# Kernel optimization log

Hardware: AMD Instinct MI355X
Metric: run time of the kernel (lower is better)

## Reference

```python
import jax, jax.numpy as jnp
import numpy as np

B, C, H, W = 4, 32, 128, 256
EPS = 1e-5  # BatchNorm eps


def _conv1x1_bn(x, w, b, gamma, beta, mean, var):
    # x: [B,C,H,W]; 1x1 conv == channel matmul, fused with eval-mode BatchNorm
    y = jnp.einsum('bchw,oc->bohw', x, w) + b[None, :, None, None]
    scale = gamma / jnp.sqrt(var + EPS)
    shift = beta - mean * scale
    return y * scale[None, :, None, None] + shift[None, :, None, None]


def setup_inputs() -> dict:
    key = jax.random.key(0)
    ks = jax.random.split(key, 15)
    d = {
        'x_left': jax.random.normal(ks[0], (B, C, H, W), jnp.float32),
        'x_right': jax.random.normal(ks[1], (B, C, H, W), jnp.float32),
        'cost': jax.random.normal(ks[2], (2, B, H, W, W), jnp.float32),
        'q_w': jax.random.normal(ks[3], (C, C), jnp.float32),
        'q_b': jax.random.normal(ks[4], (C,), jnp.float32),
        'q_gamma': jax.random.uniform(ks[5], (C,), jnp.float32),
        'q_beta': jax.random.normal(ks[6], (C,), jnp.float32),
        'q_mean': jax.random.normal(ks[7], (C,), jnp.float32),
        'q_var': jax.random.uniform(ks[8], (C,), jnp.float32),
        'k_w': jax.random.normal(ks[9], (C, C), jnp.float32),
        'k_b': jax.random.normal(ks[10], (C,), jnp.float32),
        'k_gamma': jax.random.uniform(ks[11], (C,), jnp.float32),
        'k_beta': jax.random.normal(ks[12], (C,), jnp.float32),
        'k_mean': jax.random.normal(ks[13], (C,), jnp.float32),
        'k_var': jax.random.uniform(ks[14], (C,), jnp.float32),
    }
    return d


def reference(x_left, x_right, cost, q_w, q_b, q_gamma, q_beta, q_mean, q_var,
              k_w, k_b, k_gamma, k_beta, k_mean, k_var):
    b, c, h, w = x_left.shape
    cr = w // 3  # clamped_range

    # band masks: right2left keeps 0 <= i-j < cr (lower band); left2right keeps 0 <= j-i < cr
    idx = jnp.arange(w)
    diff = idx[:, None] - idx[None, :]  # [W,W] = i - j
    low_band = ((diff >= 0) & (diff < cr)).astype(x_left.dtype)
    up_band = low_band.T

    # right-to-left: Q from left, K from right
    q_l = jnp.transpose(_conv1x1_bn(x_left, q_w, q_b, q_gamma, q_beta, q_mean, q_var), (0, 2, 3, 1))   # [B,H,W,C]
    k_r = jnp.transpose(_conv1x1_bn(x_right, k_w, k_b, k_gamma, k_beta, k_mean, k_var), (0, 2, 3, 1))  # [B,H,W,C]
    s_r2l = jnp.einsum('bhic,bhjc->bhij', q_l, k_r) / c  # [B,H,W,W]
    cost_r2l = s_r2l * low_band + cost[0]

    # left-to-right: Q from right, K from left
    q_r = jnp.transpose(_conv1x1_bn(x_right, q_w, q_b, q_gamma, q_beta, q_mean, q_var), (0, 2, 3, 1))
    k_l = jnp.transpose(_conv1x1_bn(x_left, k_w, k_b, k_gamma, k_beta, k_mean, k_var), (0, 2, 3, 1))
    s_l2r = jnp.einsum('bhic,bhjc->bhij', q_r, k_l) / c
    cost_l2r = s_l2r * up_band + cost[1]

    # original returns (x_left + fea_left, x_right + fea_right, (r2l, l2r)) with fea == x
    return (x_left * 2.0, x_right * 2.0, cost_r2l, cost_l2r)
```

## Files before the change

### kernel.cpp

```cpp
#include <hip/hip_runtime.h>

#define BB 4
#define CC 32
#define HH 128
#define WW 256
#define CR 85
#define EPSF 1e-5f

#define O1_OFF 4194304
#define O2_OFF 8388608
#define COST1 33554432

typedef __attribute__((ext_vector_type(8))) short bf16x8;
typedef __attribute__((ext_vector_type(4))) float f32x4;
typedef __attribute__((ext_vector_type(4))) float f4v;

static __device__ __forceinline__ unsigned short f2bf(float f) {
    unsigned u = __float_as_uint(f);
    unsigned r = (u + 0x7FFFu + ((u >> 16) & 1u)) >> 16;
    return (unsigned short)r;
}

__global__ __launch_bounds__(256, 3)
void pab_fused_one(const float* __restrict__ x_left, const float* __restrict__ x_right,
                   const float* __restrict__ cost,
                   const float* __restrict__ q_w, const float* __restrict__ q_b,
                   const float* __restrict__ q_gamma, const float* __restrict__ q_beta,
                   const float* __restrict__ q_mean, const float* __restrict__ q_var,
                   const float* __restrict__ k_w, const float* __restrict__ k_b,
                   const float* __restrict__ k_gamma, const float* __restrict__ k_beta,
                   const float* __restrict__ k_mean, const float* __restrict__ k_var,
                   float* __restrict__ out)
{
    __shared__ unsigned short Qs[WW * CC];
    __shared__ unsigned short Ks[WW * CC];
    __shared__ char smem[32 * 132 * 4];
    float* Sb = (float*)smem;
    float (*wqs)[CC] = (float(*)[CC])smem;
    float (*wks)[CC] = (float(*)[CC])(smem + 4096);
    float* bqs = (float*)(smem + 8192);
    float* bks = (float*)(smem + 8320);
    float* sqs = (float*)(smem + 8448);
    float* sks = (float*)(smem + 8576);

    const int t   = threadIdx.x;
    const int dir = blockIdx.x >> 9;
    const int bh  = blockIdx.x & 511;
    const int b = bh >> 7, h = bh & 127;

    if (t < CC) {
        float qs_ = q_gamma[t] * rsqrtf(q_var[t] + EPSF);
        float ks_ = k_gamma[t] * rsqrtf(k_var[t] + EPSF);
        sqs[t] = qs_; sks[t] = ks_;
        bqs[t] = q_b[t] * qs_ + q_beta[t] - q_mean[t] * qs_;
        bks[t] = k_b[t] * ks_ + k_beta[t] - k_mean[t] * ks_;
    }
    __syncthreads();
    for (int r = t; r < CC * CC; r += 256) {
        int o = r >> 5, c = r & 31;
        wqs[c][o] = q_w[r] * sqs[o];
        wks[c][o] = k_w[r] * sks[o];
    }
    __syncthreads();

    const float* xq = dir ? x_right : x_left;
    const float* xk = dir ? x_left  : x_right;
    float* outq = out + (dir ? O1_OFF : 0);
    const int xbase = (b * CC * HH + h) * WW + t;

    {
        float q[CC];
        #pragma unroll
        for (int o = 0; o < CC; ++o) q[o] = bqs[o];
        #pragma unroll 4
        for (int c = 0; c < CC; ++c) {
            int idx = xbase + c * (HH * WW);
            float xv = xq[idx];
            __builtin_nontemporal_store(2.0f * xv, outq + idx);
            #pragma unroll
            for (int o = 0; o < CC; ++o) q[o] += xv * wqs[c][o];
        }
        unsigned short* qdst = Qs + t * CC;
        #pragma unroll
        for (int g = 0; g < 4; ++g) {
            uint4 v;
            v.x = f2bf(q[8*g+0]) | ((unsigned)f2bf(q[8*g+1]) << 16);
            v.y = f2bf(q[8*g+2]) | ((unsigned)f2bf(q[8*g+3]) << 16);
            v.z = f2bf(q[8*g+4]) | ((unsigned)f2bf(q[8*g+5]) << 16);
            v.w = f2bf(q[8*g+6]) | ((unsigned)f2bf(q[8*g+7]) << 16);
            ((uint4*)qdst)[g] = v;
        }
    }
    {
        float k[CC];
        #pragma unroll
        for (int o = 0; o < CC; ++o) k[o] = bks[o];
        #pragma unroll 4
        for (int c = 0; c < CC; ++c) {
            float xv = xk[xbase + c * (HH * WW)];
            #pragma unroll
            for (int o = 0; o < CC; ++o) k[o] += xv * wks[c][o];
        }
        unsigned short* kdst = Ks + t * CC;
        #pragma unroll
        for (int g = 0; g < 4; ++g) {
            uint4 v;
            v.x = f2bf(k[8*g+0]) | ((unsigned)f2bf(k[8*g+1]) << 16);
            v.y = f2bf(k[8*g+2]) | ((unsigned)f2bf(k[8*g+3]) << 16);
            v.z = f2bf(k[8*g+4]) | ((unsigned)f2bf(k[8*g+5]) << 16);
            v.w = f2bf(k[8*g+6]) | ((unsigned)f2bf(k[8*g+7]) << 16);
            ((uint4*)kdst)[g] = v;
        }
    }
    __syncthreads();

    const float* csrc = cost + (size_t)dir * COST1 + (size_t)bh * (WW * WW);
    float* odst = out + O2_OFF + (size_t)dir * COST1 + (size_t)bh * (WW * WW);
    const int rowlane = t >> 6;
    const int c4 = 4 * (t & 63);
    const int w = t >> 6, lane = t & 63;
    const int quad = lane >> 4, l16 = lane & 15;
    const float inv32 = 1.0f / 32.0f;

    for (int tile = 0; tile < 8; ++tile) {
        const int i0 = tile * 32;
        const int wbase = dir ? i0 : (i0 - 96);

        f4v vbuf[8];
        #pragma unroll
        for (int p = 0; p < 8; ++p) {
            int rl = 4 * p + rowlane;
            vbuf[p] = __builtin_nontemporal_load((const f4v*)(csrc + (i0 + rl) * WW + c4));
        }

        bf16x8 qf[2], kf[2];
        #pragma unroll
        for (int mt = 0; mt < 2; ++mt)
            qf[mt] = *(const bf16x8*)(Qs + (i0 + 16 * mt + l16) * CC + quad * 8);
        #pragma unroll
        for (int nt = 0; nt < 2; ++nt) {
            int col = wbase + 32 * w + 16 * nt + l16;
            bf16x8 kv = {};
            if (col >= 0 && col < WW)
                kv = *(const bf16x8*)(Ks + col * CC + quad * 8);
            kf[nt] = kv;
        }

        f32x4 acc[2][2] = {};
        #pragma unroll
        for (int mt = 0; mt < 2; ++mt)
            #pragma unroll
            for (int nt = 0; nt < 2; ++nt)
                acc[mt][nt] = __builtin_amdgcn_mfma_f32_16x16x32_bf16(
                    qf[mt], kf[nt], acc[mt][nt], 0, 0, 0);

        __syncthreads();

        #pragma unroll
        for (int mt = 0; mt < 2; ++mt)
            #pragma unroll
            for (int nt = 0; nt < 2; ++nt) {
                int cl = 32 * w + 16 * nt + l16;
                #pragma unroll
                for (int r = 0; r < 4; ++r) {
                    int row = 16 * mt + quad * 4 + r;
                    Sb[row * 132 + cl] = acc[mt][nt][r];
                }
            }
        __syncthreads();

        const int lc = c4 - wbase;
        const bool inwin = (lc >= 0 && lc < 128);
        #pragma unroll
        for (int p = 0; p < 8; ++p) {
            int rl = 4 * p + rowlane;
            int i = i0 + rl;
            f4v v = vbuf[p];
            if (inwin) {
                const f4v s = *(const f4v*)(Sb + rl * 132 + lc);
                int d0 = dir ? (c4 + 0 - i) : (i - c4 - 0);
                int d1 = dir ? (c4 + 1 - i) : (i - c4 - 1);
                int d2 = dir ? (c4 + 2 - i) : (i - c4 - 2);
                int d3 = dir ? (c4 + 3 - i) : (i - c4 - 3);
                if (d0 >= 0 && d0 < CR) v[0] += s[0] * inv32;
                if (d1 >= 0 && d1 < CR) v[1] += s[1] * inv32;
                if (d2 >= 0 && d2 < CR) v[2] += s[2] * inv32;
                if (d3 >= 0 && d3 < CR) v[3] += s[3] * inv32;
            }
            __builtin_nontemporal_store(v, (f4v*)(odst + (size_t)i * WW + c4));
        }
    }
}

extern "C" void kernel_launch(void* const* d_in, const int* in_sizes, int n_in,
                              void* d_out, int out_size, void* d_ws, size_t ws_size,
                              hipStream_t stream) {
    const float* x_left  = (const float*)d_in[0];
    const float* x_right = (const float*)d_in[1];
    const float* cost    = (const float*)d_in[2];
    const float* q_w     = (const float*)d_in[3];
    const float* q_b     = (const float*)d_in[4];
    const float* q_gamma = (const float*)d_in[5];
    const float* q_beta  = (const float*)d_in[6];
    const float* q_mean  = (const float*)d_in[7];
    const float* q_var   = (const float*)d_in[8];
    const float* k_w     = (const float*)d_in[9];
    const float* k_b     = (const float*)d_in[10];
    const float* k_gamma = (const float*)d_in[11];
    const float* k_beta  = (const float*)d_in[12];
    const float* k_mean  = (const float*)d_in[13];
    const float* k_var   = (const float*)d_in[14];
    float* out = (float*)d_out;

    pab_fused_one<<<dim3(1024), dim3(256), 0, stream>>>(
        x_left, x_right, cost,
        q_w, q_b, q_gamma, q_beta, q_mean, q_var,
        k_w, k_b, k_gamma, k_beta, k_mean, k_var,
        out);
}
```

Before: 531.4 us.

## Split each row across two blocks, prefetch cost tiles, swizzle score buffer

Each (dir,b,h) row is split into two blocks, each covering 128 query rows, which doubles the grid to 2048 blocks and raises the occupancy hint to 4. The first cost tile is loaded before the Q/K projections and the next tile is prefetched inside the store loop, so global loads overlap with compute. Q projection work is split across thread halves with 16 outputs each. The score buffer uses an XOR swizzle instead of padding to avoid LDS bank conflicts. The cost is that the K projection for the full row is now recomputed by both halves.

```diff
diff --git a/kernel.cpp b/kernel.cpp
--- a/kernel.cpp
+++ b/kernel.cpp
@@ -21,20 +21,22 @@
     return (unsigned short)r;
 }
 
-__global__ __launch_bounds__(256, 3)
-void pab_fused_one(const float* __restrict__ x_left, const float* __restrict__ x_right,
-                   const float* __restrict__ cost,
-                   const float* __restrict__ q_w, const float* __restrict__ q_b,
-                   const float* __restrict__ q_gamma, const float* __restrict__ q_beta,
-                   const float* __restrict__ q_mean, const float* __restrict__ q_var,
-                   const float* __restrict__ k_w, const float* __restrict__ k_b,
-                   const float* __restrict__ k_gamma, const float* __restrict__ k_beta,
-                   const float* __restrict__ k_mean, const float* __restrict__ k_var,
-                   float* __restrict__ out)
+#define SBS(r, c) ((r) * 128 + (((((c) >> 2) ^ ((r) & 7)) << 2) | ((c) & 3)))
+
+__global__ __launch_bounds__(256, 4)
+void pab_fused_half(const float* __restrict__ x_left, const float* __restrict__ x_right,
+                    const float* __restrict__ cost,
+                    const float* __restrict__ q_w, const float* __restrict__ q_b,
+                    const float* __restrict__ q_gamma, const float* __restrict__ q_beta,
+                    const float* __restrict__ q_mean, const float* __restrict__ q_var,
+                    const float* __restrict__ k_w, const float* __restrict__ k_b,
+                    const float* __restrict__ k_gamma, const float* __restrict__ k_beta,
+                    const float* __restrict__ k_mean, const float* __restrict__ k_var,
+                    float* __restrict__ out)
 {
-    __shared__ unsigned short Qs[WW * CC];
+    __shared__ unsigned short Qs[128 * CC];
     __shared__ unsigned short Ks[WW * CC];
-    __shared__ char smem[32 * 132 * 4];
+    __shared__ char smem[32 * 128 * 4];
     float* Sb = (float*)smem;
     float (*wqs)[CC] = (float(*)[CC])smem;
     float (*wks)[CC] = (float(*)[CC])(smem + 4096);
@@ -43,10 +45,25 @@
     float* sqs = (float*)(smem + 8448);
     float* sks = (float*)(smem + 8576);
 
-    const int t   = threadIdx.x;
-    const int dir = blockIdx.x >> 9;
-    const int bh  = blockIdx.x & 511;
+    const int t    = threadIdx.x;
+    const int bx   = blockIdx.x;
+    const int dir  = bx >> 10;
+    const int bh   = (bx >> 1) & 511;
+    const int half = bx & 1;
     const int b = bh >> 7, h = bh & 127;
+    const int ibase = half * 128;
+
+    const float* csrc = cost + (size_t)dir * COST1 + (size_t)bh * (WW * WW);
+    float* odst = out + O2_OFF + (size_t)dir * COST1 + (size_t)bh * (WW * WW);
+    const int rowlane = t >> 6;
+    const int c4 = 4 * (t & 63);
+
+    f4v vbuf[8];
+    #pragma unroll
+    for (int p = 0; p < 8; ++p) {
+        int rl = 4 * p + rowlane;
+        vbuf[p] = __builtin_nontemporal_load((const f4v*)(csrc + (ibase + rl) * WW + c4));
+    }
 
     if (t < CC) {
         float qs_ = q_gamma[t] * rsqrtf(q_var[t] + EPSF);
@@ -66,38 +83,15 @@
     const float* xq = dir ? x_right : x_left;
     const float* xk = dir ? x_left  : x_right;
     float* outq = out + (dir ? O1_OFF : 0);
-    const int xbase = (b * CC * HH + h) * WW + t;
 
     {
-        float q[CC];
-        #pragma unroll
-        for (int o = 0; o < CC; ++o) q[o] = bqs[o];
+        float k[CC];
+        #pragma unroll
+        for (int o = 0; o < CC; ++o) k[o] = bks[o];
+        const int xkbase = (b * CC * HH + h) * WW + t;
         #pragma unroll 4
         for (int c = 0; c < CC; ++c) {
-            int idx = xbase + c * (HH * WW);
-            float xv = xq[idx];
-            __builtin_nontemporal_store(2.0f * xv, outq + idx);
-            #pragma unroll
-            for (int o = 0; o < CC; ++o) q[o] += xv * wqs[c][o];
-        }
-        unsigned short* qdst = Qs + t * CC;
-        #pragma unroll
-        for (int g = 0; g < 4; ++g) {
-            uint4 v;
-            v.x = f2bf(q[8*g+0]) | ((unsigned)f2bf(q[8*g+1]) << 16);
-            v.y = f2bf(q[8*g+2]) | ((unsigned)f2bf(q[8*g+3]) << 16);
-            v.z = f2bf(q[8*g+4]) | ((unsigned)f2bf(q[8*g+5]) << 16);
-            v.w = f2bf(q[8*g+6]) | ((unsigned)f2bf(q[8*g+7]) << 16);
-            ((uint4*)qdst)[g] = v;
-        }
-    }
-    {
-        float k[CC];
-        #pragma unroll
-        for (int o = 0; o < CC; ++o) k[o] = bks[o];
-        #pragma unroll 4
-        for (int c = 0; c < CC; ++c) {
-            float xv = xk[xbase + c * (HH * WW)];
+            float xv = xk[xkbase + c * (HH * WW)];
             #pragma unroll
             for (int o = 0; o < CC; ++o) k[o] += xv * wks[c][o];
         }
@@ -112,31 +106,48 @@
             ((uint4*)kdst)[g] = v;
         }
     }
+
+    {
+        const int lpx = t & 127;
+        const int oh  = t >> 7;
+        const int ob  = oh * 16;
+        float q[16];
+        #pragma unroll
+        for (int o = 0; o < 16; ++o) q[o] = bqs[ob + o];
+        const int xqbase = (b * CC * HH + h) * WW + ibase + lpx;
+        #pragma unroll 4
+        for (int c = 0; c < CC; ++c) {
+            float xv = xq[xqbase + c * (HH * WW)];
+            if (t < 128)
+                __builtin_nontemporal_store(2.0f * xv, outq + xqbase + c * (HH * WW));
+            #pragma unroll
+            for (int o = 0; o < 16; ++o) q[o] += xv * wqs[c][ob + o];
+        }
+        unsigned short* qdst = Qs + lpx * CC + ob;
+        #pragma unroll
+        for (int g = 0; g < 2; ++g) {
+            uint4 v;
+            v.x = f2bf(q[8*g+0]) | ((unsigned)f2bf(q[8*g+1]) << 16);
+            v.y = f2bf(q[8*g+2]) | ((unsigned)f2bf(q[8*g+3]) << 16);
+            v.z = f2bf(q[8*g+4]) | ((unsigned)f2bf(q[8*g+5]) << 16);
+            v.w = f2bf(q[8*g+6]) | ((unsigned)f2bf(q[8*g+7]) << 16);
+            ((uint4*)qdst)[g] = v;
+        }
+    }
     __syncthreads();
 
-    const float* csrc = cost + (size_t)dir * COST1 + (size_t)bh * (WW * WW);
-    float* odst = out + O2_OFF + (size_t)dir * COST1 + (size_t)bh * (WW * WW);
-    const int rowlane = t >> 6;
-    const int c4 = 4 * (t & 63);
     const int w = t >> 6, lane = t & 63;
     const int quad = lane >> 4, l16 = lane & 15;
     const float inv32 = 1.0f / 32.0f;
 
-    for (int tile = 0; tile < 8; ++tile) {
-        const int i0 = tile * 32;
+    for (int tt = 0; tt < 4; ++tt) {
+        const int i0 = ibase + tt * 32;
         const int wbase = dir ? i0 : (i0 - 96);
 
-        f4v vbuf[8];
-        #pragma unroll
-        for (int p = 0; p < 8; ++p) {
-            int rl = 4 * p + rowlane;
-            vbuf[p] = __builtin_nontemporal_load((const f4v*)(csrc + (i0 + rl) * WW + c4));
-        }
-
         bf16x8 qf[2], kf[2];
         #pragma unroll
         for (int mt = 0; mt < 2; ++mt)
-            qf[mt] = *(const bf16x8*)(Qs + (i0 + 16 * mt + l16) * CC + quad * 8);
+            qf[mt] = *(const bf16x8*)(Qs + (tt * 32 + 16 * mt + l16) * CC + quad * 8);
         #pragma unroll
         for (int nt = 0; nt < 2; ++nt) {
             int col = wbase + 32 * w + 16 * nt + l16;
@@ -164,7 +175,7 @@
                 #pragma unroll
                 for (int r = 0; r < 4; ++r) {
                     int row = 16 * mt + quad * 4 + r;
-                    Sb[row * 132 + cl] = acc[mt][nt][r];
+                    Sb[SBS(row, cl)] = acc[mt][nt][r];
                 }
             }
         __syncthreads();
@@ -177,7 +188,7 @@
             int i = i0 + rl;
             f4v v = vbuf[p];
             if (inwin) {
-                const f4v s = *(const f4v*)(Sb + rl * 132 + lc);
+                const f4v s = *(const f4v*)(Sb + rl * 128 + (((lc >> 2) ^ (rl & 7)) << 2));
                 int d0 = dir ? (c4 + 0 - i) : (i - c4 - 0);
                 int d1 = dir ? (c4 + 1 - i) : (i - c4 - 1);
                 int d2 = dir ? (c4 + 2 - i) : (i - c4 - 2);
@@ -188,6 +199,9 @@
                 if (d3 >= 0 && d3 < CR) v[3] += s[3] * inv32;
             }
             __builtin_nontemporal_store(v, (f4v*)(odst + (size_t)i * WW + c4));
+            if (tt < 3)
+                vbuf[p] = __builtin_nontemporal_load(
+                    (const f4v*)(csrc + (i0 + 32 + rl) * WW + c4));
         }
     }
 }
@@ -212,7 +226,7 @@
     const float* k_var   = (const float*)d_in[14];
     float* out = (float*)d_out;
 
-    pab_fused_one<<<dim3(1024), dim3(256), 0, stream>>>(
+    pab_fused_half<<<dim3(2048), dim3(256), 0, stream>>>(
         x_left, x_right, cost,
         q_w, q_b, q_gamma, q_beta, q_mean, q_var,
         k_w, k_b, k_gamma, k_beta, k_mean, k_var,
```

After: 536.8 us. About the same (+1.0%).
